# Kernel tuning notes

Hardware: AMD Instinct MI355X
Metric: run time of the kernel (lower is better)

The kernel has to match this reference:

```python
import jax, jax.numpy as jnp
import numpy as np
from jax import lax

K = 3          # kernel_size
G = 2          # num_groups
DN = ('NHWC', 'HWIO', 'NHWC')


def _conv_same(x, w, b, groups=1):
    y = lax.conv_general_dilated(x, w, (1, 1), 'SAME',
                                 dimension_numbers=DN,
                                 feature_group_count=groups)
    return y + b


def _kernel_grid():
    off = (K - 1) / 2.0
    lin = jnp.linspace(-off, off, K, dtype=jnp.float32)
    dx, dy = jnp.meshgrid(lin, lin)              # 'xy' indexing, like tf default
    return jnp.stack([dx, dy], axis=-1).reshape(K * K, 2)  # [K2, 2] (dx, dy)


def _bilinear_sample(inp, loc):
    # inp: [B,H,W,C], loc: [B,H,W,K2,2] with (x,y) already clipped to valid range
    B, H, W, C = inp.shape
    x, y = loc[..., 0], loc[..., 1]
    x0 = jnp.floor(x); y0 = jnp.floor(y)
    x1 = jnp.clip(x0 + 1.0, 0.0, W - 1.0); x0 = jnp.clip(x0, 0.0, W - 1.0)
    y1 = jnp.clip(y0 + 1.0, 0.0, H - 1.0); y0 = jnp.clip(y0, 0.0, H - 1.0)
    # corner weights (computed from clipped coords, matching the TF code)
    wa = (x1 - x) * (y1 - y)
    wb = (x1 - x) * (y - y0)
    wc = (x - x0) * (y1 - y)
    wd = (x - x0) * (y - y0)
    x0i = x0.astype(jnp.int32); x1i = x1.astype(jnp.int32)
    y0i = y0.astype(jnp.int32); y1i = y1.astype(jnp.int32)
    flat = inp.reshape(B, H * W, C)

    def gather(yi, xi):
        idx = (yi * W + xi).reshape(B, -1, 1)               # [B, H*W*K2, 1]
        v = jnp.take_along_axis(flat, idx, axis=1)          # [B, H*W*K2, C]
        return v.reshape(B, H, W, K * K, C)

    out = (wa[..., None] * gather(y0i, x0i) + wb[..., None] * gather(y1i, x0i)
           + wc[..., None] * gather(y0i, x1i) + wd[..., None] * gather(y1i, x1i))
    return out  # [B,H,W,K2,C]


def _forward(x, off_w, off_b, dw_w, dw_b, pw_w, pw_b):
    B, H, W, C = x.shape
    Cg = C // G
    kg = _kernel_grid()                                     # [K2,2]
    gx, gy = jnp.meshgrid(jnp.arange(W, dtype=jnp.float32),
                          jnp.arange(H, dtype=jnp.float32))
    grid = jnp.stack([gx, gy], axis=-1)                     # [H,W,2] (x,y)
    outs = []
    for g in range(G):
        xi = x[..., g * Cg:(g + 1) * Cg]                    # [B,H,W,Cg]
        offsets = _conv_same(xi, off_w[g], off_b[g])        # [B,H,W,2*K2]
        offsets = offsets.reshape(B, H, W, K * K, 2)
        loc = grid[None, :, :, None, :] + kg[None, None, None] + offsets
        loc = jnp.stack([jnp.clip(loc[..., 0], 0.0, W - 1.0),
                         jnp.clip(loc[..., 1], 0.0, H - 1.0)], axis=-1)
        sampled = _bilinear_sample(xi, loc)                 # [B,H,W,K2,Cg]
        Kin = K * K * Cg
        s = sampled.reshape(B, H, W, Kin)
        s = _conv_same(s, dw_w[g], dw_b[g], groups=Kin)     # depthwise 3x3
        s = _conv_same(s, pw_w[g], pw_b[g])                 # 1x1 pointwise
        outs.append(s)
    return jnp.concatenate(outs, axis=-1)


def setup_inputs() -> dict:
    key = jax.random.key(0)
    ks = jax.random.split(key, 6)
    B, H, W, C = 4, 128, 128, 128
    Cg = C // G
    F = 128
    Fg = F // G
    Kin = K * K * Cg
    x = jax.random.normal(ks[0], (B, H, W, C), jnp.float32)
    # offset conv (zero-init in source; small random weights so offsets ~1px)
    off_w = jax.random.normal(ks[1], (G, K, K, Cg, 2 * K * K), jnp.float32) * 0.05
    off_b = jnp.zeros((G, 2 * K * K), jnp.float32)
    dw_w = jax.random.normal(ks[2], (G, K, K, 1, Kin), jnp.float32) * 0.1
    dw_b = jnp.zeros((G, Kin), jnp.float32)
    pw_w = jax.random.normal(ks[3], (G, 1, 1, Kin, Fg), jnp.float32) / np.sqrt(Kin)
    pw_b = jnp.zeros((G, Fg), jnp.float32)
    return {"x": x, "off_w": off_w, "off_b": off_b,
            "dw_w": dw_w, "dw_b": dw_b, "pw_w": pw_w, "pw_b": pw_b}


def reference(x, off_w, off_b, dw_w, dw_b, pw_w, pw_b):
    return _forward(x, off_w, off_b, dw_w, dw_b, pw_w, pw_b)
```

## Files before the change

### kernel.cpp

```cpp
#include <hip/hip_runtime.h>
#include <hip/hip_bf16.h>

#define HW 128
#define GNUM 2
#define BATCH 4
#define OBT_STRIDE (GNUM * 18 * 2 * 512)
#define PWT_FLOATS 36864
#define OBT_FLOATS 36864
#define DWP_WORDS 5184

typedef short s16x8 __attribute__((ext_vector_type(8)));
typedef _Float16 f16x8 __attribute__((ext_vector_type(8)));
typedef _Float16 f16x2 __attribute__((ext_vector_type(2)));
typedef __fp16 h16x2 __attribute__((ext_vector_type(2)));
typedef float f32x4 __attribute__((ext_vector_type(4)));

__device__ inline unsigned short f2bf(float f) {
    union { float f; unsigned u; } v;
    v.f = f;
    unsigned r = (v.u + 0x7fffu + ((v.u >> 16) & 1u)) >> 16;
    return (unsigned short)r;
}
__device__ inline unsigned pk2bf(float lo, float hi) {
    __hip_bfloat162 r = __float22bfloat162_rn(float2{lo, hi});
    return *(unsigned*)&r;
}
__device__ inline float blo(unsigned u) {
    union { unsigned u; float f; } v; v.u = u << 16; return v.f;
}
__device__ inline float bhi(unsigned u) {
    union { unsigned u; float f; } v; v.u = u & 0xffff0000u; return v.f;
}
__device__ inline unsigned short f2h(float f) {
    _Float16 h = (_Float16)f;
    return *(unsigned short*)&h;
}
__device__ inline unsigned pk2h(float lo, float hi) {
    union { h16x2 h; unsigned u; } v;
    v.h = __builtin_amdgcn_cvt_pkrtz(lo, hi);
    return v.u;
}
__device__ inline f16x2 u2h(unsigned u) {
    union { unsigned u; f16x2 h; } v; v.u = u; return v.h;
}
__device__ inline unsigned h2u(f16x2 h) {
    union { unsigned u; f16x2 h; } v; v.h = h; return v.u;
}

__global__ __launch_bounds__(256) void prep_kernel(
    const float* __restrict__ pw_w, const float* __restrict__ dw_b,
    const float* __restrict__ off_w, const float* __restrict__ dw_w,
    unsigned short* __restrict__ pwt, unsigned short* __restrict__ obt,
    unsigned* __restrict__ dwp, float* __restrict__ bias2) {
    const int g = blockIdx.y;
    const int t = threadIdx.x;
    if (blockIdx.x < 9) {
        const int j = blockIdx.x;
        const int wv = t >> 6, lane = t & 63;
        const int f = wv * 16 + (lane & 15);
        const int kbase = (lane >> 4) << 3;
        float part = 0.f;
#pragma unroll
        for (int ks = 0; ks < 2; ++ks)
#pragma unroll
            for (int i = 0; i < 8; ++i) {
                int kin = j * 64 + ks * 32 + kbase + i;
                float v = pw_w[(g * 576 + kin) * 64 + f];
                pwt[((((g * 9 + j) * 4 + wv) * 2 + ks) << 9) + lane * 8 + i] =
                    f2h(v);
                part += v * dw_b[g * 576 + kin];
            }
        atomicAdd(&bias2[g * 64 + f], part);
        for (int e = t; e < 288; e += 256) {
            int tap2 = e >> 5, cp = e & 31;
            const float* dwr = &dw_w[(g * 9 + tap2) * 576 + (j << 6) + cp * 2];
            dwp[(((g * 9 + tap2) * 9 + j) << 5) + cp] = pk2h(dwr[0], dwr[1]);
        }
    } else {
        const int s = blockIdx.x - 9;
        const int tap = s >> 1;
        for (int e = t; e < 1024; e += 256) {
            int nt = e >> 9, le = e & 511;
            int lane = le >> 3, i = le & 7;
            int k = ((lane >> 4) << 3) + i;
            int c = ((s & 1) << 5) + k;
            int n = (nt << 4) + (lane & 15);
            float v = (n < 18) ? off_w[((g * 9 + tap) * 64 + c) * 18 + n] : 0.f;
            unsigned short hi = f2bf(v);
            unsigned short lo = f2bf(v - blo(hi));
            int idx = (((g * 18 + s) * 2 + nt) << 9) + le;
            obt[idx] = hi;
            obt[OBT_STRIDE + idx] = lo;
        }
    }
}

__global__ __launch_bounds__(256, 4) void deform_fused(
    const float* __restrict__ x, const unsigned short* __restrict__ obt,
    const float* __restrict__ off_b, const unsigned* __restrict__ dwp,
    const unsigned short* __restrict__ pwt, const float* __restrict__ bias2,
    const float* __restrict__ pw_b, float* __restrict__ out) {
    __shared__ char smem[34016];
    unsigned short* xh = (unsigned short*)smem;
    unsigned short* samp = (unsigned short*)smem;
    unsigned short* dwa = (unsigned short*)(smem + 14400);
    float* offs = (float*)(smem + 23616);
    float4* wlw = (float4*)(smem + 30816);
    int4* wli = (int4*)(smem + 32416);

    const int b = blockIdx.x >> 1, g = blockIdx.x & 1;
    const int tileIdx = blockIdx.y;
    const int h0 = (tileIdx >> 4) << 3, w0 = (tileIdx & 15) << 3;
    const int t = threadIdx.x;
    const int lane = t & 63;
    const int wv = __builtin_amdgcn_readfirstlane(t >> 6);
    const int kq = (lane >> 4) << 3;
    const int col = lane & 15;
    const int rq = (lane >> 4) << 2;

    f32x4 oacc[2][2];
#pragma unroll
    for (int sl = 0; sl < 2; ++sl)
#pragma unroll
        for (int nt = 0; nt < 2; ++nt) oacc[sl][nt] = (f32x4){0.f, 0.f, 0.f, 0.f};
    int mbase[2];
#pragma unroll
    for (int sl = 0; sl < 2; ++sl) {
        int mt = wv + (sl << 2);
        int m = mt * 16 + col;
        if (mt < 7 && m < 100) {
            int opy = m / 10, opx = m - opy * 10;
            mbase[sl] = opy * 12 + opx;
        } else
            mbase[sl] = 0;
    }
    for (int q = 0; q < 2; ++q) {
        if (q) __syncthreads();
        for (int idx = t; idx < 144 * 8; idx += 256) {
            int sp = idx >> 3, cq = idx & 7;
            int sy = sp / 12, sx = sp - sy * 12;
            int gy = h0 - 2 + sy, gx = w0 - 2 + sx;
            uint2 hp = {0, 0}, lp = {0, 0};
            if ((unsigned)gy < HW && (unsigned)gx < HW) {
                const float4 v = *(const float4*)&x[(((b * HW + gy) * HW + gx)
                                                    << 7) +
                                                   (g << 6) + (q << 5) + (cq << 2)];
                hp.x = pk2bf(v.x, v.y);
                hp.y = pk2bf(v.z, v.w);
                lp.x = pk2bf(v.x - blo(hp.x), v.y - bhi(hp.x));
                lp.y = pk2bf(v.z - blo(hp.y), v.w - bhi(hp.y));
            }
            *(uint2*)&xh[sp * 72 + (cq << 2)] = hp;
            *(uint2*)&xh[sp * 72 + 32 + (cq << 2)] = lp;
        }
        __syncthreads();
        for (int tap = 0; tap < 9; ++tap) {
            const int s = (tap << 1) + q;
            const int ky = tap / 3, kx = tap - ky * 3;
            const int shift = ky * 12 + kx;
            const int bidx = ((g * 18 + s) << 1) << 9;
            s16x8 bh0 = *(const s16x8*)&obt[bidx + lane * 8];
            s16x8 bh1 = *(const s16x8*)&obt[bidx + 512 + lane * 8];
            s16x8 bl0 = *(const s16x8*)&obt[OBT_STRIDE + bidx + lane * 8];
            s16x8 bl1 = *(const s16x8*)&obt[OBT_STRIDE + bidx + 512 + lane * 8];
#pragma unroll
            for (int sl = 0; sl < 2; ++sl) {
                if (wv + (sl << 2) < 7) {
                    const int base2 = (mbase[sl] + shift) * 72 + kq;
                    s16x8 ah = *(const s16x8*)&xh[base2];
                    s16x8 al = *(const s16x8*)&xh[base2 + 32];
                    oacc[sl][0] = __builtin_amdgcn_mfma_f32_16x16x32_bf16(
                        ah, bh0, oacc[sl][0], 0, 0, 0);
                    oacc[sl][1] = __builtin_amdgcn_mfma_f32_16x16x32_bf16(
                        ah, bh1, oacc[sl][1], 0, 0, 0);
                    oacc[sl][0] = __builtin_amdgcn_mfma_f32_16x16x32_bf16(
                        al, bh0, oacc[sl][0], 0, 0, 0);
                    oacc[sl][1] = __builtin_amdgcn_mfma_f32_16x16x32_bf16(
                        al, bh1, oacc[sl][1], 0, 0, 0);
                    oacc[sl][0] = __builtin_amdgcn_mfma_f32_16x16x32_bf16(
                        ah, bl0, oacc[sl][0], 0, 0, 0);
                    oacc[sl][1] = __builtin_amdgcn_mfma_f32_16x16x32_bf16(
                        ah, bl1, oacc[sl][1], 0, 0, 0);
                }
            }
        }
    }
#pragma unroll
    for (int sl = 0; sl < 2; ++sl) {
        int mt = wv + (sl << 2);
        if (mt < 7) {
#pragma unroll
            for (int nt = 0; nt < 2; ++nt) {
                int o = (nt << 4) + col;
                if (o < 18) {
                    float ob = off_b[g * 18 + o];
#pragma unroll
                    for (int i = 0; i < 4; ++i) {
                        int m = mt * 16 + rq + i;
                        if (m < 100) offs[m * 18 + o] = oacc[sl][nt][i] + ob;
                    }
                }
            }
        }
    }
    __syncthreads();

    const int fb = wv << 4;
    const int p = lane;
    const int ayp = p >> 3, axp = p & 7;
    const int grp = t >> 4, sl16 = t & 15;
    const int pbase = (ayp * 10 + axp) * 72;

    const float bs = bias2[g * 64 + fb + col] + pw_b[g * 64 + fb + col];
    f32x4 acc[4];
#pragma unroll
    for (int mt = 0; mt < 4; ++mt) acc[mt] = (f32x4){bs, bs, bs, bs};

    for (int j = 0; j < 9; ++j) {
        const int jy = j / 3, jx = j - jy * 3;
        f16x8 bfr[2];
#pragma unroll
        for (int ks = 0; ks < 2; ++ks)
            bfr[ks] = *(const f16x8*)&pwt[((((g * 9 + j) * 4 + wv) * 2 + ks)
                                           << 9) + lane * 8];
        if (t < 100) {
            const int sp = t;
            const int spy = sp / 10, spx = sp - spy * 10;
            const int gy = h0 - 1 + spy, gx = w0 - 1 + spx;
            float4 w4 = {0.f, 0.f, 0.f, 0.f};
            int4 ii = {b << 21, 0, 0, 0};
            if ((unsigned)gy < HW && (unsigned)gx < HW) {
                const float ox = offs[sp * 18 + 2 * j];
                const float oy = offs[sp * 18 + 2 * j + 1];
                float xf = fminf(fmaxf((float)(gx + jx - 1) + ox, 0.f), 127.f);
                float yf = fminf(fmaxf((float)(gy + jy - 1) + oy, 0.f), 127.f);
                float x0 = floorf(xf), y0 = floorf(yf);
                float x1 = fminf(x0 + 1.f, 127.f);
                float y1 = fminf(y0 + 1.f, 127.f);
                w4.x = (x1 - xf) * (y1 - yf);
                w4.y = (x1 - xf) * (yf - y0);
                w4.z = (xf - x0) * (y1 - yf);
                w4.w = (xf - x0) * (yf - y0);
                const int x0i = (int)x0, y0i = (int)y0;
                ii.x = ((b * HW + y0i) * HW + x0i) << 7;
                ii.y = ((int)x1 - x0i) << 7;
                ii.z = ((int)y1 - y0i) << 14;
            }
            wlw[sp] = w4;
            wli[sp] = ii;
        }
        __syncthreads();
        for (int it = 0; it < 7; ++it) {
            const int sp = (it << 4) + grp;
            if (sp < 100) {
                const float4 w4 = wlw[sp];
                const int4 ii = wli[sp];
                const float* xa = x + ii.x + (g << 6) + (sl16 << 2);
                const float4 va = *(const float4*)xa;
                const float4 vb = *(const float4*)(xa + ii.z);
                const float4 vc = *(const float4*)(xa + ii.y);
                const float4 vd = *(const float4*)(xa + ii.y + ii.z);
                float r0 = w4.x * va.x + w4.y * vb.x + w4.z * vc.x + w4.w * vd.x;
                float r1 = w4.x * va.y + w4.y * vb.y + w4.z * vc.y + w4.w * vd.y;
                float r2 = w4.x * va.z + w4.y * vb.z + w4.z * vc.z + w4.w * vd.z;
                float r3 = w4.x * va.w + w4.y * vb.w + w4.z * vc.w + w4.w * vd.w;
                uint2 pk;
                pk.x = pk2h(r0, r1);
                pk.y = pk2h(r2, r3);
                *(uint2*)&samp[sp * 72 + (sl16 << 2)] = pk;
            }
        }
        __syncthreads();
#pragma unroll
        for (int cq = 0; cq < 2; ++cq) {
            const int c8 = fb + (cq << 3);
            f16x2 d0 = {0, 0}, d1 = {0, 0}, d2 = {0, 0}, d3 = {0, 0};
#pragma unroll
            for (int t2 = 0; t2 < 9; ++t2) {
                const int ky = t2 / 3, kx = t2 - ky * 3;
                const uint4 hv =
                    *(const uint4*)&samp[pbase + (ky * 10 + kx) * 72 + c8];
                const uint4 wq =
                    *(const uint4*)&dwp[(((g * 9 + t2) * 9 + j) << 5) +
                                        (c8 >> 1)];
                d0 = u2h(hv.x) * u2h(wq.x) + d0;
                d1 = u2h(hv.y) * u2h(wq.y) + d1;
                d2 = u2h(hv.z) * u2h(wq.z) + d2;
                d3 = u2h(hv.w) * u2h(wq.w) + d3;
            }
            uint4 pk;
            pk.x = h2u(d0);
            pk.y = h2u(d1);
            pk.z = h2u(d2);
            pk.w = h2u(d3);
            *(uint4*)&dwa[p * 72 + c8] = pk;
        }
        __syncthreads();
#pragma unroll
        for (int ks = 0; ks < 2; ++ks)
#pragma unroll
            for (int mt = 0; mt < 4; ++mt) {
                f16x8 af = *(const f16x8*)&dwa[(mt * 16 + col) * 72 + ks * 32 +
                                               kq];
                acc[mt] = __builtin_amdgcn_mfma_f32_16x16x32_f16(
                    af, bfr[ks], acc[mt], 0, 0, 0);
            }
    }
#pragma unroll
    for (int mt = 0; mt < 4; ++mt)
#pragma unroll
        for (int i = 0; i < 4; ++i) {
            int m = mt * 16 + rq + i;
            out[((b * HW + h0 + (m >> 3)) * HW + (w0 + (m & 7))) * 128 +
                (g << 6) + fb + col] = acc[mt][i];
        }
}

extern "C" void kernel_launch(void* const* d_in, const int* in_sizes, int n_in,
                              void* d_out, int out_size, void* d_ws,
                              size_t ws_size, hipStream_t stream) {
    const float* x = (const float*)d_in[0];
    const float* off_w = (const float*)d_in[1];
    const float* off_b = (const float*)d_in[2];
    const float* dw_w = (const float*)d_in[3];
    const float* dw_b = (const float*)d_in[4];
    const float* pw_w = (const float*)d_in[5];
    const float* pw_b = (const float*)d_in[6];

    float* wsf = (float*)d_ws;
    unsigned short* pwt = (unsigned short*)wsf;
    unsigned short* obt = (unsigned short*)(wsf + PWT_FLOATS);
    unsigned* dwp = (unsigned*)(wsf + PWT_FLOATS + OBT_FLOATS);
    float* bias2 = wsf + PWT_FLOATS + OBT_FLOATS + DWP_WORDS;

    (void)hipMemsetAsync(bias2, 0, GNUM * 64 * sizeof(float), stream);
    prep_kernel<<<dim3(27, GNUM), dim3(256), 0, stream>>>(pw_w, dw_b, off_w,
                                                          dw_w, pwt, obt, dwp,
                                                          bias2);
    deform_fused<<<dim3(BATCH * GNUM, 256), dim3(256), 0, stream>>>(
        x, obt, off_b, dwp, pwt, bias2, pw_b, (float*)d_out);
}
```

Baseline: 200.1 us.

## Swizzle LDS rows, pack bilinear indices, shrink smem for higher occupancy

```diff
diff --git a/kernel.cpp b/kernel.cpp
--- a/kernel.cpp
+++ b/kernel.cpp
@@ -45,6 +45,9 @@
 }
 __device__ inline unsigned h2u(f16x2 h) {
     union { unsigned u; f16x2 h; } v; v.h = h; return v.u;
+}
+__device__ inline int swz(int row, int off) {
+    return (off & 7) | ((((off >> 3) ^ (row + (row >> 3))) & 7) << 3);
 }
 
 __global__ __launch_bounds__(256) void prep_kernel(
@@ -59,24 +62,20 @@
         const int wv = t >> 6, lane = t & 63;
         const int f = wv * 16 + (lane & 15);
         const int kbase = (lane >> 4) << 3;
-        float part = 0.f;
 #pragma unroll
         for (int ks = 0; ks < 2; ++ks)
 #pragma unroll
             for (int i = 0; i < 8; ++i) {
                 int kin = j * 64 + ks * 32 + kbase + i;
-                float v = pw_w[(g * 576 + kin) * 64 + f];
                 pwt[((((g * 9 + j) * 4 + wv) * 2 + ks) << 9) + lane * 8 + i] =
-                    f2h(v);
-                part += v * dw_b[g * 576 + kin];
-            }
-        atomicAdd(&bias2[g * 64 + f], part);
+                    f2h(pw_w[(g * 576 + kin) * 64 + f]);
+            }
         for (int e = t; e < 288; e += 256) {
             int tap2 = e >> 5, cp = e & 31;
             const float* dwr = &dw_w[(g * 9 + tap2) * 576 + (j << 6) + cp * 2];
             dwp[(((g * 9 + tap2) * 9 + j) << 5) + cp] = pk2h(dwr[0], dwr[1]);
         }
-    } else {
+    } else if (blockIdx.x < 27) {
         const int s = blockIdx.x - 9;
         const int tap = s >> 1;
         for (int e = t; e < 1024; e += 256) {
@@ -92,21 +91,28 @@
             obt[idx] = hi;
             obt[OBT_STRIDE + idx] = lo;
         }
-    }
-}
-
-__global__ __launch_bounds__(256, 4) void deform_fused(
+    } else {
+        if (t < 64) {
+            float s = 0.f;
+            for (int kin = 0; kin < 576; ++kin)
+                s += pw_w[(g * 576 + kin) * 64 + t] * dw_b[g * 576 + kin];
+            bias2[g * 64 + t] = s;
+        }
+    }
+}
+
+__global__ __launch_bounds__(256, 5) void deform_fused(
     const float* __restrict__ x, const unsigned short* __restrict__ obt,
     const float* __restrict__ off_b, const unsigned* __restrict__ dwp,
     const unsigned short* __restrict__ pwt, const float* __restrict__ bias2,
     const float* __restrict__ pw_b, float* __restrict__ out) {
-    __shared__ char smem[34016];
+    __shared__ char smem[30192];
     unsigned short* xh = (unsigned short*)smem;
     unsigned short* samp = (unsigned short*)smem;
-    unsigned short* dwa = (unsigned short*)(smem + 14400);
-    float* offs = (float*)(smem + 23616);
-    float4* wlw = (float4*)(smem + 30816);
-    int4* wli = (int4*)(smem + 32416);
+    unsigned short* dwa = (unsigned short*)(smem + 12800);
+    float* offs = (float*)(smem + 20992);
+    float4* wlw = (float4*)(smem + 28192);
+    unsigned* wli = (unsigned*)(smem + 29792);
 
     const int b = blockIdx.x >> 1, g = blockIdx.x & 1;
     const int tileIdx = blockIdx.y;
@@ -150,8 +156,8 @@
                 lp.x = pk2bf(v.x - blo(hp.x), v.y - bhi(hp.x));
                 lp.y = pk2bf(v.z - blo(hp.y), v.w - bhi(hp.y));
             }
-            *(uint2*)&xh[sp * 72 + (cq << 2)] = hp;
-            *(uint2*)&xh[sp * 72 + 32 + (cq << 2)] = lp;
+            *(uint2*)&xh[sp * 64 + swz(sp, cq << 2)] = hp;
+            *(uint2*)&xh[sp * 64 + swz(sp, 32 + (cq << 2))] = lp;
         }
         __syncthreads();
         for (int tap = 0; tap < 9; ++tap) {
@@ -166,9 +172,9 @@
 #pragma unroll
             for (int sl = 0; sl < 2; ++sl) {
                 if (wv + (sl << 2) < 7) {
-                    const int base2 = (mbase[sl] + shift) * 72 + kq;
-                    s16x8 ah = *(const s16x8*)&xh[base2];
-                    s16x8 al = *(const s16x8*)&xh[base2 + 32];
+                    const int m2 = mbase[sl] + shift;
+                    s16x8 ah = *(const s16x8*)&xh[m2 * 64 + swz(m2, kq)];
+                    s16x8 al = *(const s16x8*)&xh[m2 * 64 + swz(m2, kq + 32)];
                     oacc[sl][0] = __builtin_amdgcn_mfma_f32_16x16x32_bf16(
                         ah, bh0, oacc[sl][0], 0, 0, 0);
                     oacc[sl][1] = __builtin_amdgcn_mfma_f32_16x16x32_bf16(
@@ -209,7 +215,7 @@
     const int p = lane;
     const int ayp = p >> 3, axp = p & 7;
     const int grp = t >> 4, sl16 = t & 15;
-    const int pbase = (ayp * 10 + axp) * 72;
+    const int prow = ayp * 10 + axp;
 
     const float bs = bias2[g * 64 + fb + col] + pw_b[g * 64 + fb + col];
     f32x4 acc[4];
@@ -228,7 +234,7 @@
             const int spy = sp / 10, spx = sp - spy * 10;
             const int gy = h0 - 1 + spy, gx = w0 - 1 + spx;
             float4 w4 = {0.f, 0.f, 0.f, 0.f};
-            int4 ii = {b << 21, 0, 0, 0};
+            unsigned wp = (unsigned)(b << 21);
             if ((unsigned)gy < HW && (unsigned)gx < HW) {
                 const float ox = offs[sp * 18 + 2 * j];
                 const float oy = offs[sp * 18 + 2 * j + 1];
@@ -242,24 +248,27 @@
                 w4.z = (xf - x0) * (y1 - yf);
                 w4.w = (xf - x0) * (yf - y0);
                 const int x0i = (int)x0, y0i = (int)y0;
-                ii.x = ((b * HW + y0i) * HW + x0i) << 7;
-                ii.y = ((int)x1 - x0i) << 7;
-                ii.z = ((int)y1 - y0i) << 14;
+                wp = (unsigned)(((b * HW + y0i) * HW + x0i) << 7) |
+                     (unsigned)((int)x1 - x0i) |
+                     ((unsigned)((int)y1 - y0i) << 1);
             }
             wlw[sp] = w4;
-            wli[sp] = ii;
+            wli[sp] = wp;
         }
         __syncthreads();
         for (int it = 0; it < 7; ++it) {
             const int sp = (it << 4) + grp;
             if (sp < 100) {
                 const float4 w4 = wlw[sp];
-                const int4 ii = wli[sp];
-                const float* xa = x + ii.x + (g << 6) + (sl16 << 2);
+                const unsigned wp = wli[sp];
+                const float* xa = x + (wp & 0xFFFFFF80u) + (g << 6) +
+                                  (sl16 << 2);
+                const int xo = (int)((wp & 1u) << 7);
+                const int yo = (int)((wp & 2u) << 13);
                 const float4 va = *(const float4*)xa;
-                const float4 vb = *(const float4*)(xa + ii.z);
-                const float4 vc = *(const float4*)(xa + ii.y);
-                const float4 vd = *(const float4*)(xa + ii.y + ii.z);
+                const float4 vb = *(const float4*)(xa + yo);
+                const float4 vc = *(const float4*)(xa + xo);
+                const float4 vd = *(const float4*)(xa + xo + yo);
                 float r0 = w4.x * va.x + w4.y * vb.x + w4.z * vc.x + w4.w * vd.x;
                 float r1 = w4.x * va.y + w4.y * vb.y + w4.z * vc.y + w4.w * vd.y;
                 float r2 = w4.x * va.z + w4.y * vb.z + w4.z * vc.z + w4.w * vd.z;
@@ -267,7 +276,7 @@
                 uint2 pk;
                 pk.x = pk2h(r0, r1);
                 pk.y = pk2h(r2, r3);
-                *(uint2*)&samp[sp * 72 + (sl16 << 2)] = pk;
+                *(uint2*)&samp[sp * 64 + swz(sp, sl16 << 2)] = pk;
             }
         }
         __syncthreads();
@@ -278,8 +287,9 @@
 #pragma unroll
             for (int t2 = 0; t2 < 9; ++t2) {
                 const int ky = t2 / 3, kx = t2 - ky * 3;
+                const int row = prow + ky * 10 + kx;
                 const uint4 hv =
-                    *(const uint4*)&samp[pbase + (ky * 10 + kx) * 72 + c8];
+                    *(const uint4*)&samp[row * 64 + swz(row, c8)];
                 const uint4 wq =
                     *(const uint4*)&dwp[(((g * 9 + t2) * 9 + j) << 5) +
                                         (c8 >> 1)];
@@ -293,15 +303,16 @@
             pk.y = h2u(d1);
             pk.z = h2u(d2);
             pk.w = h2u(d3);
-            *(uint4*)&dwa[p * 72 + c8] = pk;
+            *(uint4*)&dwa[p * 64 + swz(p, c8)] = pk;
         }
         __syncthreads();
 #pragma unroll
         for (int ks = 0; ks < 2; ++ks)
 #pragma unroll
             for (int mt = 0; mt < 4; ++mt) {
-                f16x8 af = *(const f16x8*)&dwa[(mt * 16 + col) * 72 + ks * 32 +
-                                               kq];
+                const int row = mt * 16 + col;
+                f16x8 af = *(const f16x8*)&dwa[row * 64 +
+                                               swz(row, ks * 32 + kq)];
                 acc[mt] = __builtin_amdgcn_mfma_f32_16x16x32_f16(
                     af, bfr[ks], acc[mt], 0, 0, 0);
             }
@@ -333,8 +344,7 @@
     unsigned* dwp = (unsigned*)(wsf + PWT_FLOATS + OBT_FLOATS);
     float* bias2 = wsf + PWT_FLOATS + OBT_FLOATS + DWP_WORDS;
 
-    (void)hipMemsetAsync(bias2, 0, GNUM * 64 * sizeof(float), stream);
-    prep_kernel<<<dim3(27, GNUM), dim3(256), 0, stream>>>(pw_w, dw_b, off_w,
+    prep_kernel<<<dim3(28, GNUM), dim3(256), 0, stream>>>(pw_w, dw_b, off_w,
                                                           dw_w, pwt, obt, dwp,
                                                           bias2);
     deform_fused<<<dim3(BATCH * GNUM, 256), dim3(256), 0, stream>>>(
```

New measurement: 266.1 us. 1.33x slower.
